# Kernel tuning notes

Hardware: AMD Instinct MI355X
Metric: run time of the kernel (lower is better)

The kernel has to match this reference:

```python
import jax, jax.numpy as jnp
import numpy as np

N = 240000
STRIDE = 4
M = N // STRIDE
C_IN = 32
C_OUT = 64
NSAMPLE = 10  # self.nsample hard-coded to 10 in __init__
MSSC = (1, 2, 4)
K3 = MSSC[2] * NSAMPLE  # 40
EPS = 1e-5


def setup_inputs() -> dict:
    key = jax.random.key(0)
    ks = jax.random.split(key, 10)
    d_in = 3 + C_IN
    s = 1.0 / np.sqrt(d_in)
    s2 = 1.0 / np.sqrt(3 * C_OUT)
    inp = {
        "p": jax.random.normal(ks[0], (N, 3), jnp.float32),
        "x": jax.random.normal(ks[1], (N, C_IN), jnp.float32),
        "o": jnp.array([N], jnp.int32),
        "fps_idx": jax.random.randint(ks[2], (M,), 0, N, dtype=jnp.int32),
        "knn_idx": jax.random.randint(ks[3], (M, K3), 0, N, dtype=jnp.int32),
        "w1": jax.random.uniform(ks[4], (d_in, C_OUT), jnp.float32, -s, s),
        "w2": jax.random.uniform(ks[5], (d_in, C_OUT), jnp.float32, -s, s),
        "w3": jax.random.uniform(ks[6], (d_in, C_OUT), jnp.float32, -s, s),
        "w": jax.random.uniform(ks[7], (3 * C_OUT, C_OUT), jnp.float32, -s2, s2),
        "b": jax.random.uniform(ks[8], (C_OUT,), jnp.float32, -s2, s2),
        "g1": jnp.ones((C_OUT,), jnp.float32),
        "g2": jnp.ones((C_OUT,), jnp.float32),
        "g3": jnp.ones((C_OUT,), jnp.float32),
        "g": jnp.ones((C_OUT,), jnp.float32),
        "be1": jnp.zeros((C_OUT,), jnp.float32),
        "be2": jnp.zeros((C_OUT,), jnp.float32),
        "be3": jnp.zeros((C_OUT,), jnp.float32),
        "be": jnp.zeros((C_OUT,), jnp.float32),
    }
    return inp


def _bn(h, gamma, beta):
    # BatchNorm1d in training mode: per-channel stats over all non-channel axes.
    axes = tuple(range(h.ndim - 1))
    mu = jnp.mean(h, axis=axes, keepdims=True)
    var = jnp.var(h, axis=axes, keepdims=True)
    return (h - mu) * jax.lax.rsqrt(var + EPS) * gamma + beta


def _branch(feat, k, w_s, gamma, beta):
    # linear (no bias) -> BN -> ReLU -> max-pool over k nearest neighbors
    h = jnp.einsum('mkc,co->mko', feat[:, :k], w_s)  # [M,k,O]
    h = jax.nn.relu(_bn(h, gamma, beta))
    return jnp.max(h, axis=1)  # [M,O]


def reference(p, x, o, fps_idx, knn_idx, w1, w2, w3, w, b,
              g1, g2, g3, g, be1, be2, be3, be):
    n_p = p[fps_idx]                                   # [M,3] FPS-sampled centroids
    rel = p[knn_idx] - n_p[:, None, :]                 # [M,K3,3] relative xyz (with_xyz=True)
    feat = jnp.concatenate([rel, x[knn_idx]], axis=-1) # [M,K3,3+C_IN]
    y = jnp.concatenate([
        _branch(feat, MSSC[0] * NSAMPLE, w1, g1, be1),
        _branch(feat, MSSC[1] * NSAMPLE, w2, g2, be2),
        _branch(feat, MSSC[2] * NSAMPLE, w3, g3, be3),
    ], axis=-1)                                        # [M,3*O]
    y = jax.nn.relu(_bn(y @ w + b, g, be))             # [M,O]
    n_o = jnp.array([M], jnp.int32)
    return n_p, y, n_o
```

## Files before the change

kernel.cpp:

```cpp
#include <hip/hip_runtime.h>
#include <hip/hip_bf16.h>

#define K3   40
#define CO   64
#define GM   16
#define CK   20
#define SROW 72
#define FS   200
#define BN_EPS 1e-5f

typedef __attribute__((ext_vector_type(8))) short short8;
typedef __attribute__((ext_vector_type(4))) float f32x4;

static __device__ __forceinline__ short f2bf(float f) {
  union { __hip_bfloat16 b; short s; } u; u.b = __float2bfloat16(f); return u.s;
}
static __device__ __forceinline__ unsigned pk2(float a, float b) {
  union { __hip_bfloat16 b; unsigned short s; } ua, ub;
  ua.b = __float2bfloat16(a); ub.b = __float2bfloat16(b);
  return (unsigned)ua.s | ((unsigned)ub.s << 16);
}


__global__ void k_init(float* __restrict__ stats, float* __restrict__ out_no, int M)
{
  int t = threadIdx.x;
  if (t < 512) stats[t] = 0.f;
  if (t == 0) out_no[0] = (float)M;
}

__global__ void __launch_bounds__(256) k_branch(
    const float* __restrict__ p, const float* __restrict__ x,
    const int* __restrict__ fps, const int* __restrict__ knn,
    const float* __restrict__ w1, const float* __restrict__ w2,
    const float* __restrict__ w3,
    float* __restrict__ hmax1, float* __restrict__ hmax2,
    float* __restrict__ hmax3,
    float* __restrict__ stats, int M)
{
  __shared__ __align__(16) short abuf[CK * GM * SROW];

  const int tid  = threadIdx.x;
  const int wv   = tid >> 6;
  const int lane = tid & 63;
  const int q    = lane >> 4;
  const int nn   = lane & 15;
  const int cg   = wv * 16 + nn;

  short8 bw1[2], bw2[2], bw3[2];
#pragma unroll
  for (int s = 0; s < 2; ++s) {
#pragma unroll
    for (int j = 0; j < 8; ++j) {
      int d = s * 32 + q * 8 + j;
      int row = (d < 32) ? (3 + d) : ((d < 35) ? (d - 32) : -1);
      bw1[s][j] = f2bf(row >= 0 ? w1[row * CO + cg] : 0.f);
      bw2[s][j] = f2bf(row >= 0 ? w2[row * CO + cg] : 0.f);
      bw3[s][j] = f2bf(row >= 0 ? w3[row * CO + cg] : 0.f);
    }
  }

  float s1b0 = 0.f, s1b1 = 0.f, s1b2 = 0.f;
  float s2b0 = 0.f, s2b1 = 0.f, s2b2 = 0.f;

  const int ngrp = M / GM;
  for (int grp = blockIdx.x; grp < ngrp; grp += gridDim.x) {
    const int base = grp * GM;
    float mx1[4], mx2[4], mx3[4];
#pragma unroll
    for (int r = 0; r < 4; ++r) { mx1[r] = -3.4e38f; mx2[r] = -3.4e38f; mx3[r] = -3.4e38f; }

    for (int ch = 0; ch < 2; ++ch) {
      __syncthreads();
      for (int r = tid; r < CK * GM; r += 256) {
        int kl = r >> 4;
        int ml = r & 15;
        int m  = base + ml;
        int k  = ch * CK + kl;
        int gi = knn[m * K3 + k];
        int fi = fps[m];
        const float4* xr = (const float4*)(x + (size_t)gi * 32);
        float4 x0 = xr[0], x1 = xr[1], x2 = xr[2], x3 = xr[3];
        float4 x4 = xr[4], x5 = xr[5], x6 = xr[6], x7 = xr[7];
        float r0 = p[gi * 3 + 0] - p[fi * 3 + 0];
        float r1 = p[gi * 3 + 1] - p[fi * 3 + 1];
        float r2 = p[gi * 3 + 2] - p[fi * 3 + 2];
        uint4 A0 = make_uint4(pk2(x0.x, x0.y), pk2(x0.z, x0.w), pk2(x1.x, x1.y), pk2(x1.z, x1.w));
        uint4 A1 = make_uint4(pk2(x2.x, x2.y), pk2(x2.z, x2.w), pk2(x3.x, x3.y), pk2(x3.z, x3.w));
        uint4 A2 = make_uint4(pk2(x4.x, x4.y), pk2(x4.z, x4.w), pk2(x5.x, x5.y), pk2(x5.z, x5.w));
        uint4 A3 = make_uint4(pk2(x6.x, x6.y), pk2(x6.z, x6.w), pk2(x7.x, x7.y), pk2(x7.z, x7.w));
        uint4 A4 = make_uint4(pk2(r0, r1), pk2(r2, 0.f), 0u, 0u);
        uint4 Z0 = make_uint4(0u, 0u, 0u, 0u);
        uint4* dst = (uint4*)&abuf[r * SROW];
        dst[0] = A0; dst[1] = A1; dst[2] = A2; dst[3] = A3;
        dst[4] = A4; dst[5] = Z0; dst[6] = Z0; dst[7] = Z0;
      }
      __syncthreads();
      for (int kl = 0; kl < CK; ++kl) {
        int kg = ch * CK + kl;
        const short* ar = &abuf[(kl * GM + nn) * SROW + q * 8];
        short8 a0 = *(const short8*)ar;
        short8 a1 = *(const short8*)(ar + 32);
        f32x4 zz = {0.f, 0.f, 0.f, 0.f};
        f32x4 h3 = __builtin_amdgcn_mfma_f32_16x16x32_bf16(a0, bw3[0], zz, 0, 0, 0);
        h3 = __builtin_amdgcn_mfma_f32_16x16x32_bf16(a1, bw3[1], h3, 0, 0, 0);
#pragma unroll
        for (int r = 0; r < 4; ++r) {
          float h = h3[r];
          mx3[r] = fmaxf(mx3[r], h); s1b2 += h; s2b2 = fmaf(h, h, s2b2);
        }
        if (kg < 20) {
          f32x4 h2 = __builtin_amdgcn_mfma_f32_16x16x32_bf16(a0, bw2[0], zz, 0, 0, 0);
          h2 = __builtin_amdgcn_mfma_f32_16x16x32_bf16(a1, bw2[1], h2, 0, 0, 0);
#pragma unroll
          for (int r = 0; r < 4; ++r) {
            float h = h2[r];
            mx2[r] = fmaxf(mx2[r], h); s1b1 += h; s2b1 = fmaf(h, h, s2b1);
          }
          if (kg < 10) {
            f32x4 h1 = __builtin_amdgcn_mfma_f32_16x16x32_bf16(a0, bw1[0], zz, 0, 0, 0);
            h1 = __builtin_amdgcn_mfma_f32_16x16x32_bf16(a1, bw1[1], h1, 0, 0, 0);
#pragma unroll
            for (int r = 0; r < 4; ++r) {
              float h = h1[r];
              mx1[r] = fmaxf(mx1[r], h); s1b0 += h; s2b0 = fmaf(h, h, s2b0);
            }
          }
        }
      }
    }
#pragma unroll
    for (int r = 0; r < 4; ++r) {
      int m = base + q * 4 + r;
      hmax1[(size_t)m * CO + cg] = mx1[r];
      hmax2[(size_t)m * CO + cg] = mx2[r];
      hmax3[(size_t)m * CO + cg] = mx3[r];
    }
  }

  {
    float v;
    v = s1b0; v += __shfl_xor(v, 16); v += __shfl_xor(v, 32);
    if (q == 0) atomicAdd(&stats[0 * 64 + cg], v);
    v = s1b1; v += __shfl_xor(v, 16); v += __shfl_xor(v, 32);
    if (q == 0) atomicAdd(&stats[1 * 64 + cg], v);
    v = s1b2; v += __shfl_xor(v, 16); v += __shfl_xor(v, 32);
    if (q == 0) atomicAdd(&stats[2 * 64 + cg], v);
    v = s2b0; v += __shfl_xor(v, 16); v += __shfl_xor(v, 32);
    if (q == 0) atomicAdd(&stats[192 + 0 * 64 + cg], v);
    v = s2b1; v += __shfl_xor(v, 16); v += __shfl_xor(v, 32);
    if (q == 0) atomicAdd(&stats[192 + 1 * 64 + cg], v);
    v = s2b2; v += __shfl_xor(v, 16); v += __shfl_xor(v, 32);
    if (q == 0) atomicAdd(&stats[192 + 2 * 64 + cg], v);
  }
}

__global__ void k_bn_branch(const float* __restrict__ stats,
                            const float* __restrict__ g1, const float* __restrict__ g2,
                            const float* __restrict__ g3,
                            const float* __restrict__ be1, const float* __restrict__ be2,
                            const float* __restrict__ be3,
                            float* __restrict__ bnp, int M)
{
  int t = threadIdx.x;
  if (t >= 192) return;
  int b = t >> 6, c = t & 63;
  float cnt = (float)M * (float)(10 << b);
  float mu  = stats[t] / cnt;
  float var = stats[192 + t] / cnt - mu * mu;
  const float* g  = (b == 0) ? g1 : ((b == 1) ? g2 : g3);
  const float* be = (b == 0) ? be1 : ((b == 1) ? be2 : be3);
  float sc = g[c] * rsqrtf(var + BN_EPS);
  bnp[t] = sc;
  bnp[192 + t] = be[c] - mu * sc;
}

__global__ void __launch_bounds__(256) k_fuse(
    const float* __restrict__ hmax1, const float* __restrict__ hmax2,
    const float* __restrict__ hmax3,
    const float* __restrict__ bnp, const float* __restrict__ w,
    const float* __restrict__ bias,
    const float* __restrict__ p, const int* __restrict__ fps,
    float* __restrict__ zout, float* __restrict__ stats,
    float* __restrict__ out_np, int M)
{
  __shared__ __align__(16) short ybuf[GM * FS];

  const int tid  = threadIdx.x;
  const int wv   = tid >> 6;
  const int lane = tid & 63;
  const int q    = lane >> 4;
  const int nn   = lane & 15;
  const int cg   = wv * 16 + nn;

  short8 bw[6];
#pragma unroll
  for (int s = 0; s < 6; ++s)
#pragma unroll
    for (int j = 0; j < 8; ++j)
      bw[s][j] = f2bf(w[(s * 32 + q * 8 + j) * CO + cg]);

  const float bia = bias[cg];
  float s1 = 0.f, s2 = 0.f;

  const int ml_s = tid >> 4;
  const int c4   = (tid & 15) * 4;

  const int ngrp = M / GM;
  for (int grp = blockIdx.x; grp < ngrp; grp += gridDim.x) {
    const int base = grp * GM;
#pragma unroll
    for (int b = 0; b < 3; ++b) {
      const float* hb = (b == 0) ? hmax1 : ((b == 1) ? hmax2 : hmax3);
      float4 v  = *(const float4*)&hb[(size_t)(base + ml_s) * CO + c4];
      float4 sc = *(const float4*)&bnp[b * 64 + c4];
      float4 sh = *(const float4*)&bnp[192 + b * 64 + c4];
      float y0 = fmaxf(fmaf(v.x, sc.x, sh.x), 0.f);
      float y1 = fmaxf(fmaf(v.y, sc.y, sh.y), 0.f);
      float y2 = fmaxf(fmaf(v.z, sc.z, sh.z), 0.f);
      float y3 = fmaxf(fmaf(v.w, sc.w, sh.w), 0.f);
      *(uint2*)&ybuf[ml_s * FS + b * 64 + c4] = make_uint2(pk2(y0, y1), pk2(y2, y3));
    }
    if (tid < 48) {
      int ml2 = tid / 3, d = tid - ml2 * 3;
      int fi = fps[base + ml2];
      out_np[(size_t)(base + ml2) * 3 + d] = p[fi * 3 + d];
    }
    __syncthreads();
    const short* ar = &ybuf[nn * FS + q * 8];
    f32x4 acc = {0.f, 0.f, 0.f, 0.f};
#pragma unroll
    for (int s = 0; s < 6; ++s) {
      short8 a = *(const short8*)(ar + s * 32);
      acc = __builtin_amdgcn_mfma_f32_16x16x32_bf16(a, bw[s], acc, 0, 0, 0);
    }
#pragma unroll
    for (int r = 0; r < 4; ++r) {
      float z = acc[r] + bia;
      int m = base + q * 4 + r;
      zout[(size_t)m * CO + cg] = z;
      s1 += z; s2 = fmaf(z, z, s2);
    }
    __syncthreads();
  }

  float v;
  v = s1; v += __shfl_xor(v, 16); v += __shfl_xor(v, 32);
  if (q == 0) atomicAdd(&stats[384 + cg], v);
  v = s2; v += __shfl_xor(v, 16); v += __shfl_xor(v, 32);
  if (q == 0) atomicAdd(&stats[448 + cg], v);
}

__global__ void k_bn_final(const float* __restrict__ stats,
                           const float* __restrict__ g, const float* __restrict__ be,
                           float* __restrict__ bnp, int M)
{
  int c = threadIdx.x;
  if (c >= 64) return;
  float mu  = stats[384 + c] / (float)M;
  float var = stats[448 + c] / (float)M - mu * mu;
  float sc = g[c] * rsqrtf(var + BN_EPS);
  bnp[384 + c] = sc;
  bnp[448 + c] = be[c] - mu * sc;
}

__global__ void k_out(float* __restrict__ y, const float* __restrict__ bnp,
                      float* __restrict__ out_no, int M)
{
  int tid = blockIdx.x * blockDim.x + threadIdx.x;
  int total = M * 64;
  if (tid < total) {
    int c = tid & 63;
    float v = fmaf(y[tid], bnp[384 + c], bnp[448 + c]);
    y[tid] = fmaxf(v, 0.f);
  }
  if (tid == 0) out_no[0] = (float)M;
}

extern "C" void kernel_launch(void* const* d_in, const int* in_sizes, int n_in,
                              void* d_out, int out_size, void* d_ws, size_t ws_size,
                              hipStream_t stream) {
  const float* p   = (const float*)d_in[0];
  const float* x   = (const float*)d_in[1];
  const int*   fps = (const int*)d_in[3];
  const int*   knn = (const int*)d_in[4];
  const float* w1  = (const float*)d_in[5];
  const float* w2  = (const float*)d_in[6];
  const float* w3  = (const float*)d_in[7];
  const float* w   = (const float*)d_in[8];
  const float* b   = (const float*)d_in[9];
  const float* g1  = (const float*)d_in[10];
  const float* g2  = (const float*)d_in[11];
  const float* g3  = (const float*)d_in[12];
  const float* g   = (const float*)d_in[13];
  const float* be1 = (const float*)d_in[14];
  const float* be2 = (const float*)d_in[15];
  const float* be3 = (const float*)d_in[16];
  const float* be  = (const float*)d_in[17];

  const int M = in_sizes[3];

  float* ws    = (float*)d_ws;
  float* hmax1 = ws;
  float* hmax2 = hmax1 + (size_t)M * 64;
  float* hmax3 = hmax2 + (size_t)M * 64;
  float* stats = hmax3 + (size_t)M * 64;
  float* bnp   = stats + 512;

  float* out    = (float*)d_out;
  float* out_np = out;
  float* out_y  = out + (size_t)3 * M;
  float* out_no = out + (size_t)67 * M;

  k_init<<<1, 512, 0, stream>>>(stats, out_no, M);
  k_branch<<<768, 256, 0, stream>>>(p, x, fps, knn, w1, w2, w3,
                                    hmax1, hmax2, hmax3, stats, M);
  k_bn_branch<<<1, 256, 0, stream>>>(stats, g1, g2, g3, be1, be2, be3, bnp, M);
  k_fuse<<<1024, 256, 0, stream>>>(hmax1, hmax2, hmax3, bnp, w, b, p, fps,
                                   out_y, stats, out_np, M);
  k_bn_final<<<1, 64, 0, stream>>>(stats, g, be, bnp, M);
  int total = M * 64;
  k_out<<<(total + 255) / 256, 256, 0, stream>>>(out_y, bnp, out_no, M);
}
```

Before: 261.4 us.

## Pre-convert features to bf16, store branch maxima in bf16, fold BN kernels

A new prologue kernel converts x to bf16 once, writes the sampled centroids, and zeroes the stats. The gather kernel then loads half the bytes per neighbor, uses a smaller LDS row and skips the zero-padding MFMA loads for most lanes. Branch max outputs are stored as bf16, which halves the intermediate traffic, and the two BN-parameter kernels are folded into their consumers. Grid sizes change so each group maps to one block, and the final pass is vectorized to float4. The extra full pass over x and the bf16 rounding of the intermediates trade some accuracy and bandwidth for cheaper gathers.

```diff
diff --git a/kernel.cpp b/kernel.cpp
--- a/kernel.cpp
+++ b/kernel.cpp
@@ -5,7 +5,7 @@
 #define CO   64
 #define GM   16
 #define CK   20
-#define SROW 72
+#define SROW 40
 #define FS   200
 #define BN_EPS 1e-5f
 
@@ -20,25 +20,50 @@
   ua.b = __float2bfloat16(a); ub.b = __float2bfloat16(b);
   return (unsigned)ua.s | ((unsigned)ub.s << 16);
 }
-
-
-__global__ void k_init(float* __restrict__ stats, float* __restrict__ out_no, int M)
+static __device__ __forceinline__ float bf2f(unsigned s) {
+  union { float f; unsigned u; } u; u.u = (s & 0xffffu) << 16; return u.f;
+}
+
+
+__global__ void __launch_bounds__(256) k_pre(
+    const float* __restrict__ p, const float* __restrict__ x,
+    const int* __restrict__ fps,
+    __hip_bfloat16* __restrict__ xb, float* __restrict__ out_np,
+    float* __restrict__ out_no, float* __restrict__ stats, int N, int M)
 {
-  int t = threadIdx.x;
-  if (t < 512) stats[t] = 0.f;
-  if (t == 0) out_no[0] = (float)M;
+  const int gid = blockIdx.x * blockDim.x + threadIdx.x;
+  const int stride = gridDim.x * blockDim.x;
+  for (int r = gid; r < N; r += stride) {
+    const float4* src = (const float4*)(x + (size_t)r * 32);
+    float4 a0 = src[0], a1 = src[1], a2 = src[2], a3 = src[3];
+    float4 a4 = src[4], a5 = src[5], a6 = src[6], a7 = src[7];
+    uint4* dst = (uint4*)(xb + (size_t)r * 32);
+    dst[0] = make_uint4(pk2(a0.x,a0.y), pk2(a0.z,a0.w), pk2(a1.x,a1.y), pk2(a1.z,a1.w));
+    dst[1] = make_uint4(pk2(a2.x,a2.y), pk2(a2.z,a2.w), pk2(a3.x,a3.y), pk2(a3.z,a3.w));
+    dst[2] = make_uint4(pk2(a4.x,a4.y), pk2(a4.z,a4.w), pk2(a5.x,a5.y), pk2(a5.z,a5.w));
+    dst[3] = make_uint4(pk2(a6.x,a6.y), pk2(a6.z,a6.w), pk2(a7.x,a7.y), pk2(a7.z,a7.w));
+  }
+  if (gid < M) {
+    int fi = fps[gid];
+    out_np[(size_t)gid * 3 + 0] = p[fi * 3 + 0];
+    out_np[(size_t)gid * 3 + 1] = p[fi * 3 + 1];
+    out_np[(size_t)gid * 3 + 2] = p[fi * 3 + 2];
+  }
+  if (gid < 512) stats[gid] = 0.f;
+  if (gid == 0) out_no[0] = (float)M;
 }
 
 __global__ void __launch_bounds__(256) k_branch(
-    const float* __restrict__ p, const float* __restrict__ x,
-    const int* __restrict__ fps, const int* __restrict__ knn,
+    const float* __restrict__ p, const __hip_bfloat16* __restrict__ xb,
+    const int* __restrict__ knn, const float* __restrict__ np,
     const float* __restrict__ w1, const float* __restrict__ w2,
     const float* __restrict__ w3,
-    float* __restrict__ hmax1, float* __restrict__ hmax2,
-    float* __restrict__ hmax3,
+    __hip_bfloat16* __restrict__ hm1, __hip_bfloat16* __restrict__ hm2,
+    __hip_bfloat16* __restrict__ hm3,
     float* __restrict__ stats, int M)
 {
   __shared__ __align__(16) short abuf[CK * GM * SROW];
+  __shared__ float npb[GM * 3];
 
   const int tid  = threadIdx.x;
   const int wv   = tid >> 6;
@@ -66,6 +91,8 @@
   const int ngrp = M / GM;
   for (int grp = blockIdx.x; grp < ngrp; grp += gridDim.x) {
     const int base = grp * GM;
+    if (tid < 48) npb[tid] = np[(size_t)base * 3 + tid];
+
     float mx1[4], mx2[4], mx3[4];
 #pragma unroll
     for (int r = 0; r < 4; ++r) { mx1[r] = -3.4e38f; mx2[r] = -3.4e38f; mx3[r] = -3.4e38f; }
@@ -75,32 +102,23 @@
       for (int r = tid; r < CK * GM; r += 256) {
         int kl = r >> 4;
         int ml = r & 15;
-        int m  = base + ml;
-        int k  = ch * CK + kl;
-        int gi = knn[m * K3 + k];
-        int fi = fps[m];
-        const float4* xr = (const float4*)(x + (size_t)gi * 32);
-        float4 x0 = xr[0], x1 = xr[1], x2 = xr[2], x3 = xr[3];
-        float4 x4 = xr[4], x5 = xr[5], x6 = xr[6], x7 = xr[7];
-        float r0 = p[gi * 3 + 0] - p[fi * 3 + 0];
-        float r1 = p[gi * 3 + 1] - p[fi * 3 + 1];
-        float r2 = p[gi * 3 + 2] - p[fi * 3 + 2];
-        uint4 A0 = make_uint4(pk2(x0.x, x0.y), pk2(x0.z, x0.w), pk2(x1.x, x1.y), pk2(x1.z, x1.w));
-        uint4 A1 = make_uint4(pk2(x2.x, x2.y), pk2(x2.z, x2.w), pk2(x3.x, x3.y), pk2(x3.z, x3.w));
-        uint4 A2 = make_uint4(pk2(x4.x, x4.y), pk2(x4.z, x4.w), pk2(x5.x, x5.y), pk2(x5.z, x5.w));
-        uint4 A3 = make_uint4(pk2(x6.x, x6.y), pk2(x6.z, x6.w), pk2(x7.x, x7.y), pk2(x7.z, x7.w));
-        uint4 A4 = make_uint4(pk2(r0, r1), pk2(r2, 0.f), 0u, 0u);
-        uint4 Z0 = make_uint4(0u, 0u, 0u, 0u);
+        int gi = knn[(base + ml) * K3 + ch * CK + kl];
+        const uint4* xr = (const uint4*)(xb + (size_t)gi * 32);
+        uint4 X0 = xr[0], X1 = xr[1], X2 = xr[2], X3 = xr[3];
+        float r0 = p[gi * 3 + 0] - npb[ml * 3 + 0];
+        float r1 = p[gi * 3 + 1] - npb[ml * 3 + 1];
+        float r2 = p[gi * 3 + 2] - npb[ml * 3 + 2];
         uint4* dst = (uint4*)&abuf[r * SROW];
-        dst[0] = A0; dst[1] = A1; dst[2] = A2; dst[3] = A3;
-        dst[4] = A4; dst[5] = Z0; dst[6] = Z0; dst[7] = Z0;
+        dst[0] = X0; dst[1] = X1; dst[2] = X2; dst[3] = X3;
+        dst[4] = make_uint4(pk2(r0, r1), pk2(r2, 0.f), 0u, 0u);
       }
       __syncthreads();
       for (int kl = 0; kl < CK; ++kl) {
         int kg = ch * CK + kl;
         const short* ar = &abuf[(kl * GM + nn) * SROW + q * 8];
         short8 a0 = *(const short8*)ar;
-        short8 a1 = *(const short8*)(ar + 32);
+        short8 a1 = {0, 0, 0, 0, 0, 0, 0, 0};
+        if (q == 0) a1 = *(const short8*)(ar + 32);
         f32x4 zz = {0.f, 0.f, 0.f, 0.f};
         f32x4 h3 = __builtin_amdgcn_mfma_f32_16x16x32_bf16(a0, bw3[0], zz, 0, 0, 0);
         h3 = __builtin_amdgcn_mfma_f32_16x16x32_bf16(a1, bw3[1], h3, 0, 0, 0);
@@ -132,9 +150,9 @@
 #pragma unroll
     for (int r = 0; r < 4; ++r) {
       int m = base + q * 4 + r;
-      hmax1[(size_t)m * CO + cg] = mx1[r];
-      hmax2[(size_t)m * CO + cg] = mx2[r];
-      hmax3[(size_t)m * CO + cg] = mx3[r];
+      hm1[(size_t)m * CO + cg] = __float2bfloat16(mx1[r]);
+      hm2[(size_t)m * CO + cg] = __float2bfloat16(mx2[r]);
+      hm3[(size_t)m * CO + cg] = __float2bfloat16(mx3[r]);
     }
   }
 
@@ -155,36 +173,18 @@
   }
 }
 
-__global__ void k_bn_branch(const float* __restrict__ stats,
-                            const float* __restrict__ g1, const float* __restrict__ g2,
-                            const float* __restrict__ g3,
-                            const float* __restrict__ be1, const float* __restrict__ be2,
-                            const float* __restrict__ be3,
-                            float* __restrict__ bnp, int M)
-{
-  int t = threadIdx.x;
-  if (t >= 192) return;
-  int b = t >> 6, c = t & 63;
-  float cnt = (float)M * (float)(10 << b);
-  float mu  = stats[t] / cnt;
-  float var = stats[192 + t] / cnt - mu * mu;
-  const float* g  = (b == 0) ? g1 : ((b == 1) ? g2 : g3);
-  const float* be = (b == 0) ? be1 : ((b == 1) ? be2 : be3);
-  float sc = g[c] * rsqrtf(var + BN_EPS);
-  bnp[t] = sc;
-  bnp[192 + t] = be[c] - mu * sc;
-}
-
 __global__ void __launch_bounds__(256) k_fuse(
-    const float* __restrict__ hmax1, const float* __restrict__ hmax2,
-    const float* __restrict__ hmax3,
-    const float* __restrict__ bnp, const float* __restrict__ w,
-    const float* __restrict__ bias,
-    const float* __restrict__ p, const int* __restrict__ fps,
-    float* __restrict__ zout, float* __restrict__ stats,
-    float* __restrict__ out_np, int M)
+    const __hip_bfloat16* __restrict__ hm1, const __hip_bfloat16* __restrict__ hm2,
+    const __hip_bfloat16* __restrict__ hm3,
+    const float* __restrict__ w, const float* __restrict__ bias,
+    const float* __restrict__ g1, const float* __restrict__ g2,
+    const float* __restrict__ g3,
+    const float* __restrict__ be1, const float* __restrict__ be2,
+    const float* __restrict__ be3,
+    float* __restrict__ zout, float* __restrict__ stats, int M)
 {
   __shared__ __align__(16) short ybuf[GM * FS];
+  __shared__ float bnl[384];
 
   const int tid  = threadIdx.x;
   const int wv   = tid >> 6;
@@ -193,6 +193,18 @@
   const int nn   = lane & 15;
   const int cg   = wv * 16 + nn;
 
+  if (tid < 192) {
+    int b = tid >> 6, c = tid & 63;
+    float cnt = (float)M * (float)(10 << b);
+    float mu  = stats[tid] / cnt;
+    float var = stats[192 + tid] / cnt - mu * mu;
+    const float* gg = (b == 0) ? g1 : ((b == 1) ? g2 : g3);
+    const float* bb = (b == 0) ? be1 : ((b == 1) ? be2 : be3);
+    float sc = gg[c] * rsqrtf(var + BN_EPS);
+    bnl[tid] = sc;
+    bnl[192 + tid] = bb[c] - mu * sc;
+  }
+
   short8 bw[6];
 #pragma unroll
   for (int s = 0; s < 6; ++s)
@@ -205,26 +217,22 @@
 
   const int ml_s = tid >> 4;
   const int c4   = (tid & 15) * 4;
+  __syncthreads();
 
   const int ngrp = M / GM;
   for (int grp = blockIdx.x; grp < ngrp; grp += gridDim.x) {
     const int base = grp * GM;
 #pragma unroll
     for (int b = 0; b < 3; ++b) {
-      const float* hb = (b == 0) ? hmax1 : ((b == 1) ? hmax2 : hmax3);
-      float4 v  = *(const float4*)&hb[(size_t)(base + ml_s) * CO + c4];
-      float4 sc = *(const float4*)&bnp[b * 64 + c4];
-      float4 sh = *(const float4*)&bnp[192 + b * 64 + c4];
-      float y0 = fmaxf(fmaf(v.x, sc.x, sh.x), 0.f);
-      float y1 = fmaxf(fmaf(v.y, sc.y, sh.y), 0.f);
-      float y2 = fmaxf(fmaf(v.z, sc.z, sh.z), 0.f);
-      float y3 = fmaxf(fmaf(v.w, sc.w, sh.w), 0.f);
+      const __hip_bfloat16* hb = (b == 0) ? hm1 : ((b == 1) ? hm2 : hm3);
+      uint2 v = *(const uint2*)&hb[(size_t)(base + ml_s) * CO + c4];
+      float4 sc = *(const float4*)&bnl[b * 64 + c4];
+      float4 sh = *(const float4*)&bnl[192 + b * 64 + c4];
+      float y0 = fmaxf(fmaf(bf2f(v.x),       sc.x, sh.x), 0.f);
+      float y1 = fmaxf(fmaf(bf2f(v.x >> 16), sc.y, sh.y), 0.f);
+      float y2 = fmaxf(fmaf(bf2f(v.y),       sc.z, sh.z), 0.f);
+      float y3 = fmaxf(fmaf(bf2f(v.y >> 16), sc.w, sh.w), 0.f);
       *(uint2*)&ybuf[ml_s * FS + b * 64 + c4] = make_uint2(pk2(y0, y1), pk2(y2, y3));
-    }
-    if (tid < 48) {
-      int ml2 = tid / 3, d = tid - ml2 * 3;
-      int fi = fps[base + ml2];
-      out_np[(size_t)(base + ml2) * 3 + d] = p[fi * 3 + d];
     }
     __syncthreads();
     const short* ar = &ybuf[nn * FS + q * 8];
@@ -251,30 +259,32 @@
   if (q == 0) atomicAdd(&stats[448 + cg], v);
 }
 
-__global__ void k_bn_final(const float* __restrict__ stats,
-                           const float* __restrict__ g, const float* __restrict__ be,
-                           float* __restrict__ bnp, int M)
+__global__ void __launch_bounds__(256) k_out(
+    float* __restrict__ y, const float* __restrict__ stats,
+    const float* __restrict__ g, const float* __restrict__ be, int M)
 {
-  int c = threadIdx.x;
-  if (c >= 64) return;
-  float mu  = stats[384 + c] / (float)M;
-  float var = stats[448 + c] / (float)M - mu * mu;
-  float sc = g[c] * rsqrtf(var + BN_EPS);
-  bnp[384 + c] = sc;
-  bnp[448 + c] = be[c] - mu * sc;
-}
-
-__global__ void k_out(float* __restrict__ y, const float* __restrict__ bnp,
-                      float* __restrict__ out_no, int M)
-{
-  int tid = blockIdx.x * blockDim.x + threadIdx.x;
-  int total = M * 64;
-  if (tid < total) {
-    int c = tid & 63;
-    float v = fmaf(y[tid], bnp[384 + c], bnp[448 + c]);
-    y[tid] = fmaxf(v, 0.f);
-  }
-  if (tid == 0) out_no[0] = (float)M;
+  __shared__ float scl[64], shl[64];
+  int tid = threadIdx.x;
+  if (tid < 64) {
+    float mu  = stats[384 + tid] / (float)M;
+    float var = stats[448 + tid] / (float)M - mu * mu;
+    float sc = g[tid] * rsqrtf(var + BN_EPS);
+    scl[tid] = sc;
+    shl[tid] = be[tid] - mu * sc;
+  }
+  __syncthreads();
+  int e0 = (blockIdx.x * blockDim.x + tid) * 4;
+  if (e0 < M * 64) {
+    int c0 = e0 & 63;
+    float4 v  = *(float4*)&y[e0];
+    float4 sc = *(float4*)&scl[c0];
+    float4 sh = *(float4*)&shl[c0];
+    v.x = fmaxf(fmaf(v.x, sc.x, sh.x), 0.f);
+    v.y = fmaxf(fmaf(v.y, sc.y, sh.y), 0.f);
+    v.z = fmaxf(fmaf(v.z, sc.z, sh.z), 0.f);
+    v.w = fmaxf(fmaf(v.w, sc.w, sh.w), 0.f);
+    *(float4*)&y[e0] = v;
+  }
 }
 
 extern "C" void kernel_launch(void* const* d_in, const int* in_sizes, int n_in,
@@ -299,26 +309,26 @@
   const float* be  = (const float*)d_in[17];
 
   const int M = in_sizes[3];
-
-  float* ws    = (float*)d_ws;
-  float* hmax1 = ws;
-  float* hmax2 = hmax1 + (size_t)M * 64;
-  float* hmax3 = hmax2 + (size_t)M * 64;
-  float* stats = hmax3 + (size_t)M * 64;
-  float* bnp   = stats + 512;
+  const int N = in_sizes[0] / 3;
+
+  char* wsb = (char*)d_ws;
+  float* stats = (float*)wsb;
+  __hip_bfloat16* xb  = (__hip_bfloat16*)(wsb + 2048);
+  __hip_bfloat16* hm1 = xb + (size_t)N * 32;
+  __hip_bfloat16* hm2 = hm1 + (size_t)M * 64;
+  __hip_bfloat16* hm3 = hm2 + (size_t)M * 64;
 
   float* out    = (float*)d_out;
   float* out_np = out;
   float* out_y  = out + (size_t)3 * M;
   float* out_no = out + (size_t)67 * M;
 
-  k_init<<<1, 512, 0, stream>>>(stats, out_no, M);
-  k_branch<<<768, 256, 0, stream>>>(p, x, fps, knn, w1, w2, w3,
-                                    hmax1, hmax2, hmax3, stats, M);
-  k_bn_branch<<<1, 256, 0, stream>>>(stats, g1, g2, g3, be1, be2, be3, bnp, M);
-  k_fuse<<<1024, 256, 0, stream>>>(hmax1, hmax2, hmax3, bnp, w, b, p, fps,
-                                   out_y, stats, out_np, M);
-  k_bn_final<<<1, 64, 0, stream>>>(stats, g, be, bnp, M);
-  int total = M * 64;
-  k_out<<<(total + 255) / 256, 256, 0, stream>>>(out_y, bnp, out_no, M);
-}
+  k_pre<<<1024, 256, 0, stream>>>(p, x, fps, xb, out_np, out_no, stats, N, M);
+  k_branch<<<1875, 256, 0, stream>>>(p, xb, knn, out_np, w1, w2, w3,
+                                     hm1, hm2, hm3, stats, M);
+  k_fuse<<<1875, 256, 0, stream>>>(hm1, hm2, hm3, w, b,
+                                   g1, g2, g3, be1, be2, be3,
+                                   out_y, stats, M);
+  int nblk = (M * 64 / 4 + 255) / 256;
+  k_out<<<nblk, 256, 0, stream>>>(out_y, stats, g, be, M);
+}
```

Measured after the change: 348.5 us. +33.3%, slower.
